# Kernel optimization log

Hardware: AMD Instinct MI355X
Metric: run time of the kernel (lower is better)

Reference implementation:

```python
import jax, jax.numpy as jnp
import numpy as np

C = 256
H = 8
D = C // H
B = 8
Q_PER = 128
KV_PER = 1024
NQ = B * Q_PER
NKV = B * KV_PER
NEG = -10000.0
MASK_EPS = 1e-6
RMS_EPS = float(np.finfo(np.float32).eps)  # torch RMSNorm default eps=None -> finfo eps


def _rms(x, w):
    return x * jax.lax.rsqrt(jnp.mean(x * x, axis=-1, keepdims=True) + RMS_EPS) * w


def _mlp(x, w1, b1, w2, b2):
    h = jax.nn.gelu(x @ w1.T + b1, approximate=False)  # torch nn.GELU is exact
    return h @ w2.T + b2


def _sdpa(qh, kh, vh, mask, scale):
    # qh [H, Nq, D], kh/vh [H, Nk, D], mask [Nq, Nk] additive
    s = jnp.einsum('hqd,hkd->hqk', qh, kh) * scale + mask[None]
    return jnp.einsum('hqk,hkd->hqd', jax.nn.softmax(s, axis=-1), vh)


def _heads(x):
    return x.reshape(-1, H, D).transpose(1, 0, 2)  # [H, N, D]


def setup_inputs() -> dict:
    key = jax.random.key(0)
    ks = jax.random.split(key, 24)
    s = 0.02
    lin = lambda k, o, i: jax.random.normal(k, (o, i), jnp.float32) * s
    inp = {
        'q': jax.random.normal(ks[0], (NQ, C), jnp.float32),
        'kv': jax.random.normal(ks[1], (NKV, C), jnp.float32),
        'cu_seqlens_q': jnp.arange(B + 1, dtype=jnp.int32) * Q_PER,
        'cu_seqlens_kv': jnp.arange(B + 1, dtype=jnp.int32) * KV_PER,
        'w_norm_kv': jnp.ones((C,), jnp.float32),
        'w_norm1': jnp.ones((C,), jnp.float32),
        'w_norm2': jnp.ones((C,), jnp.float32),
        'w_norm3': jnp.ones((C,), jnp.float32),
        'wq_c': lin(ks[2], C, C), 'wk_c': lin(ks[3], C, C), 'wv_c': lin(ks[4], C, C),
        'wo_c': lin(ks[5], C, C), 'bo_c': jnp.zeros((C,), jnp.float32),
        'wq_s': lin(ks[6], C, C), 'wkv_s': lin(ks[7], 2 * C, C),
        'wo_s': lin(ks[8], C, C), 'bo_s': jnp.zeros((C,), jnp.float32),
        'w1_mlp': lin(ks[9], 4 * C, C), 'b1_mlp': jnp.zeros((4 * C,), jnp.float32),
        'w2_mlp': lin(ks[10], C, 4 * C), 'b2_mlp': jnp.zeros((C,), jnp.float32),
        'w1_mask': lin(ks[11], C, C), 'b1_mask': jnp.zeros((C,), jnp.float32),
        'w2_mask': lin(ks[12], C, C), 'b2_mask': jnp.zeros((C,), jnp.float32),
    }
    return inp


def reference(q, kv, cu_seqlens_q, cu_seqlens_kv, w_norm_kv, w_norm1, w_norm2, w_norm3,
              wq_c, wk_c, wv_c, wo_c, bo_c, wq_s, wkv_s, wo_s, bo_s,
              w1_mlp, b1_mlp, w2_mlp, b2_mlp, w1_mask, b1_mask, w2_mask, b2_mask):
    scale = D ** (-0.5)
    nq, nkv = q.shape[0], kv.shape[0]
    # segment id per packed token from cu_seqlens
    seg_q = jnp.searchsorted(cu_seqlens_q, jnp.arange(nq), side='right') - 1
    seg_kv = jnp.searchsorted(cu_seqlens_kv, jnp.arange(nkv), side='right') - 1

    kv_n = _rms(kv, w_norm_kv)

    # mask MLP -> predicted attention mask (logits z), detached log-prob mask
    m_k = _mlp(q, w1_mask, b1_mask, w2_mask, b2_mask)          # [Nq, C]
    z = m_k @ kv_n.T                                           # [Nq, Nkv]
    p_hat = jax.nn.sigmoid(z)
    same = seg_q[:, None] == seg_kv[None, :]
    attn_mask = jnp.where(same, jnp.log(jax.lax.stop_gradient(p_hat) + MASK_EPS), NEG)

    # cross-attention (pre-norm)
    q_n = _rms(q, w_norm1)
    feat = _sdpa(_heads(q_n @ wq_c.T), _heads(kv_n @ wk_c.T), _heads(kv_n @ wv_c.T),
                 attn_mask, scale)
    feat = feat.transpose(1, 0, 2).reshape(-1, C) @ wo_c.T + bo_c
    q = q + feat

    # block-diagonal self-attention over queries
    q_n = _rms(q, w_norm2)
    kv_proj = (q_n @ wkv_s.T).reshape(-1, 2, H, D)
    self_mask = jnp.where(seg_q[:, None] == seg_q[None, :], 0.0, NEG)
    feat = _sdpa(_heads(q_n @ wq_s.T),
                 kv_proj[:, 0].transpose(1, 0, 2), kv_proj[:, 1].transpose(1, 0, 2),
                 self_mask, scale)
    feat = feat.transpose(1, 0, 2).reshape(-1, C) @ wo_s.T + bo_s
    q = q + feat

    # MLP
    q = q + _mlp(_rms(q, w_norm3), w1_mlp, b1_mlp, w2_mlp, b2_mlp)
    return q
```

## Files before the change

### kernel.cpp

```cpp
#include <hip/hip_runtime.h>
#include <math.h>


#define SCALE_ATTN 0.17677669529663687f
#define RMS_EPS 1.1920929e-07f

typedef __attribute__((ext_vector_type(8))) short bh8;
typedef __attribute__((ext_vector_type(4))) float f32x4;

__device__ __forceinline__ float bf2f(unsigned short s) {
  union { float f; unsigned u; } v; v.u = ((unsigned)s) << 16; return v.f;
}
__device__ __forceinline__ unsigned short f2bf(float f) {
  union { float f; unsigned u; } v; v.f = f;
  unsigned r = v.u + 0x7FFFu + ((v.u >> 16) & 1u);
  return (unsigned short)(r >> 16);
}
__device__ __forceinline__ unsigned pack2bf(float a, float b) {
  union { float f; unsigned u; } x, y; x.f = a; y.f = b;
  return ((x.u + 0x8000u) >> 16) | ((y.u + 0x8000u) & 0xFFFF0000u);
}
__device__ __forceinline__ float gelu_exact(float x) {
  return 0.5f * x * (1.0f + erff(x * 0.70710678118654752440f));
}

struct WP { const float* p[12]; };
__global__ __launch_bounds__(256) void k_pre(
    WP wp, unsigned short* __restrict__ wbf, unsigned short* __restrict__ w2t,
    const float* __restrict__ wn1, const float* __restrict__ wn2,
    const float* __restrict__ wn3,
    const float* __restrict__ kv, const float* __restrict__ wnkv,
    const float* __restrict__ b2m, unsigned short* __restrict__ kv_n,
    float* __restrict__ tvec, unsigned short* __restrict__ q_n,
    float* __restrict__ ssq2, float* __restrict__ ssq3) {
  int bid = blockIdx.x, tid = threadIdx.x;
  if (bid < 1408) {
    long g = ((long)bid * 256 + tid) * 4;
    const float* src; long l;
    if (g < 327680)       { src = wp.p[g >> 16]; l = g & 65535; }
    else if (g < 458752)  { src = wp.p[5];  l = g - 327680; }
    else if (g < 524288)  { src = wp.p[6];  l = g - 458752; }
    else if (g < 786432)  { src = wp.p[7];  l = g - 524288; }
    else if (g < 1048576) { src = wp.p[8];  l = g - 786432; }
    else if (g < 1114112) { src = wp.p[9];  l = g - 1048576; }
    else if (g < 1179648) { src = wp.p[10]; l = g - 1114112; }
    else                  { src = wp.p[11]; l = g - 1179648; }
    float4 v = *(const float4*)(src + l);
    if (g >= 262144 && g < 458752) {
      int k = (int)(g & 255);
      v.x *= wn2[k]; v.y *= wn2[k + 1]; v.z *= wn2[k + 2]; v.w *= wn2[k + 3];
    } else if (g >= 524288 && g < 786432) {
      int k = (int)(g & 255);
      v.x *= wn3[k]; v.y *= wn3[k + 1]; v.z *= wn3[k + 2]; v.w *= wn3[k + 3];
    }
    ushort4 o;
    o.x = f2bf(v.x); o.y = f2bf(v.y); o.z = f2bf(v.z); o.w = f2bf(v.w);
    *(ushort4*)(wbf + g) = o;
  } else if (bid < 1424) {
    __shared__ float Ts[64][65];
    int t = bid - 1408, ti = t >> 2, tj = t & 3;
    const float* w2src = wp.p[10];
    int rr = tid >> 2;
#pragma unroll
    for (int j = 0; j < 4; ++j) {
      int cc = (tid & 3) * 16 + j * 4;
      float4 v = *(const float4*)(w2src + (long)(ti * 64 + rr) * 256 + tj * 64 + cc);
      Ts[rr][cc] = v.x; Ts[rr][cc + 1] = v.y;
      Ts[rr][cc + 2] = v.z; Ts[rr][cc + 3] = v.w;
    }
    __syncthreads();
#pragma unroll
    for (int j = 0; j < 4; ++j) {
      int kk = (tid & 3) * 16 + j * 4;
      ushort4 o;
      o.x = f2bf(Ts[kk][rr]); o.y = f2bf(Ts[kk + 1][rr]);
      o.z = f2bf(Ts[kk + 2][rr]); o.w = f2bf(Ts[kk + 3][rr]);
      *(ushort4*)(w2t + (long)(tj * 64 + rr) * 256 + ti * 64 + kk) = o;
    }
  } else if (bid < 3472) {
    int row = (bid - 1424) * 4 + (tid >> 6);
    int c4 = (tid & 63) * 4;
    float4 v = *(const float4*)(kv + (long)row * 256 + c4);
    float s = v.x * v.x + v.y * v.y + v.z * v.z + v.w * v.w;
#pragma unroll
    for (int off = 32; off > 0; off >>= 1) s += __shfl_xor(s, off, 64);
    float inv = rsqrtf(s * (1.0f / 256.0f) + RMS_EPS);
    float4 wn = *(const float4*)(wnkv + c4);
    float4 b2 = *(const float4*)(b2m + c4);
    float4 vn;
    vn.x = v.x * inv * wn.x; vn.y = v.y * inv * wn.y;
    vn.z = v.z * inv * wn.z; vn.w = v.w * inv * wn.w;
    ushort4 o;
    o.x = f2bf(vn.x); o.y = f2bf(vn.y); o.z = f2bf(vn.z); o.w = f2bf(vn.w);
    *(ushort4*)(kv_n + (long)row * 256 + c4) = o;
    float s2 = vn.x * b2.x + vn.y * b2.y + vn.z * b2.z + vn.w * b2.w;
#pragma unroll
    for (int off = 32; off > 0; off >>= 1) s2 += __shfl_xor(s2, off, 64);
    if ((tid & 63) == 0) tvec[row] = s2;
  } else if (bid < 3728) {
    int row = (bid - 3472) * 4 + (tid >> 6);
    int c4 = (tid & 63) * 4;
    const float* q = wp.p[11];
    float4 v = *(const float4*)(q + (long)row * 256 + c4);
    float s = v.x * v.x + v.y * v.y + v.z * v.z + v.w * v.w;
#pragma unroll
    for (int off = 32; off > 0; off >>= 1) s += __shfl_xor(s, off, 64);
    float inv = rsqrtf(s * (1.0f / 256.0f) + RMS_EPS);
    float4 wn = *(const float4*)(wn1 + c4);
    ushort4 o;
    o.x = f2bf(v.x * inv * wn.x); o.y = f2bf(v.y * inv * wn.y);
    o.z = f2bf(v.z * inv * wn.z); o.w = f2bf(v.w * inv * wn.w);
    *(ushort4*)(q_n + (long)row * 256 + c4) = o;
  } else {
    int idx = (bid - 3728) * 256 + tid;
    if (idx < 1024) ssq2[idx] = 0.f;
    else if (idx < 2048) ssq3[idx - 1024] = 0.f;
  }
}

template <int MT, int KS>
__device__ __forceinline__ void gemm_core(
    const unsigned short* __restrict__ A, const unsigned short* __restrict__ W,
    const float* bias, const float* R, const float* ssqIn, float* ssqOut,
    float* Cf, unsigned short* Cb, unsigned short* Cb2,
    int lda, int ldw, int ldc, int m0, int n0, int epi) {
  int tid = threadIdx.x, w = tid >> 6, lane = tid & 63;
  int quad = lane >> 4, c = lane & 15;
  __shared__ __align__(16) unsigned short As[2][MT * 64][40];
  __shared__ __align__(16) unsigned short Ws[2][64][40];
  f32x4 acc[MT][4];
#pragma unroll
  for (int i = 0; i < MT; ++i)
#pragma unroll
    for (int j = 0; j < 4; ++j) acc[i][j] = (f32x4){0.f, 0.f, 0.f, 0.f};
  int ar = tid >> 2, ak = (tid & 3) * 8;
  {
    int4 a0 = *(const int4*)(A + (long)(m0 + ar) * lda + ak);
    int4 a1;
    if (MT == 2) a1 = *(const int4*)(A + (long)(m0 + 64 + ar) * lda + ak);
    int4 wv = *(const int4*)(W + (long)(n0 + ar) * ldw + ak);
    *(int4*)&As[0][ar][ak] = a0;
    if (MT == 2) *(int4*)&As[0][64 + ar][ak] = a1;
    *(int4*)&Ws[0][ar][ak] = wv;
  }
  __syncthreads();
#pragma unroll
  for (int i = 0; i < KS; ++i) {
    int cur = i & 1, nxt = cur ^ 1;
    int4 na0, na1, nwv;
    if (i + 1 < KS) {
      int k0 = (i + 1) * 32;
      na0 = *(const int4*)(A + (long)(m0 + ar) * lda + k0 + ak);
      if (MT == 2)
        na1 = *(const int4*)(A + (long)(m0 + 64 + ar) * lda + k0 + ak);
      nwv = *(const int4*)(W + (long)(n0 + ar) * ldw + k0 + ak);
    }
    bh8 af[MT];
#pragma unroll
    for (int mt = 0; mt < MT; ++mt)
      af[mt] = *(const bh8*)&As[cur][w * (16 * MT) + mt * 16 + c][quad * 8];
#pragma unroll
    for (int nt = 0; nt < 4; ++nt) {
      bh8 bf = *(const bh8*)&Ws[cur][nt * 16 + c][quad * 8];
#pragma unroll
      for (int mt = 0; mt < MT; ++mt)
        acc[mt][nt] =
            __builtin_amdgcn_mfma_f32_16x16x32_bf16(af[mt], bf, acc[mt][nt], 0, 0, 0);
    }
    if (i + 1 < KS) {
      *(int4*)&As[nxt][ar][ak] = na0;
      if (MT == 2) *(int4*)&As[nxt][64 + ar][ak] = na1;
      *(int4*)&Ws[nxt][ar][ak] = nwv;
      __syncthreads();
    }
  }
  float rsum[MT][4];
#pragma unroll
  for (int mt = 0; mt < MT; ++mt)
#pragma unroll
    for (int r = 0; r < 4; ++r) rsum[mt][r] = 0.f;
#pragma unroll
  for (int mt = 0; mt < MT; ++mt)
#pragma unroll
    for (int nt = 0; nt < 4; ++nt)
#pragma unroll
      for (int r = 0; r < 4; ++r) {
        int m = m0 + w * (16 * MT) + mt * 16 + quad * 4 + r;
        int n = n0 + nt * 16 + c;
        float v = acc[mt][nt][r];
        long ci = (long)m * ldc + n;
        if (epi == 1) {
          if (bias) v += bias[n];
          Cb[ci] = f2bf(gelu_exact(v));
        } else if (epi == 5) {
          Cb[ci] = f2bf(v);
        } else if (epi == 3) {
          if (bias) v += bias[n];
          Cb[ci] = f2bf(1.0f / (1.0f + __expf(-v)) + 1e-6f);
        } else if (epi == 2) {
          if (bias) v += bias[n];
          v += R[ci];
          Cf[ci] = v;
          if (Cb2) Cb2[ci] = f2bf(v);
          rsum[mt][r] += v * v;
        } else if (epi == 6) {
          v *= rsqrtf(ssqIn[m] * (1.0f / 256.0f) + RMS_EPS);
          if (bias) v += bias[n];
          Cb[ci] = f2bf(gelu_exact(v));
        } else {
          v *= rsqrtf(ssqIn[m] * (1.0f / 256.0f) + RMS_EPS);
          Cb[ci] = f2bf(v);
        }
      }
  if (epi == 2 && ssqOut) {
#pragma unroll
    for (int mt = 0; mt < MT; ++mt)
#pragma unroll
      for (int r = 0; r < 4; ++r) {
        float s = rsum[mt][r];
        s += __shfl_xor(s, 1, 64);
        s += __shfl_xor(s, 2, 64);
        s += __shfl_xor(s, 4, 64);
        s += __shfl_xor(s, 8, 64);
        if (c == 0)
          atomicAdd(&ssqOut[m0 + w * (16 * MT) + mt * 16 + quad * 4 + r], s);
      }
  }
}

template <int MT, int KS>
__global__ __launch_bounds__(256) void k_gemm(
    const unsigned short* A, const unsigned short* W,
    const float* bias, long sBh, const float* R,
    const float* ssqIn, float* ssqOut,
    float* Cf, unsigned short* Cb, unsigned short* Cb2,
    int lda, int ldw, int ldc, long sAh, long sWh, long sCh, int epi) {
  int z = blockIdx.z;
  long coff = (long)z * sCh;
  gemm_core<MT, KS>(A + (long)z * sAh, W + (long)z * sWh,
                    bias ? bias + (long)z * sBh : nullptr, R, ssqIn, ssqOut,
                    Cf ? Cf + coff : nullptr, Cb ? Cb + coff : nullptr, Cb2,
                    lda, ldw, ldc, blockIdx.y * (MT * 64), blockIdx.x * 64, epi);
}

struct G4 {
  const unsigned short* A; const unsigned short* W;
  const float* bias; float* Cf; unsigned short* Cb;
  int lda, ldw, ldc, epi, nx, blkStart;
};
struct G4x { G4 g[4]; };
__global__ __launch_bounds__(256) void k_gemm4(G4x d) {
  int z = blockIdx.x;
  int i = 3;
  while (i > 0 && z < d.g[i].blkStart) --i;
  const G4& g = d.g[i];
  int local = z - g.blkStart;
  int by = local / g.nx, bx = local - by * g.nx;
  gemm_core<2, 8>(g.A, g.W, g.bias, nullptr, nullptr, nullptr,
                  g.Cf, g.Cb, nullptr, g.lda, g.ldw, g.ldc,
                  by * 128, bx * 64, g.epi);
}

__global__ __launch_bounds__(256) void k_gemm_cmb(
    const float* __restrict__ partL, const float* __restrict__ partO,
    const unsigned short* __restrict__ W, const float* __restrict__ bias,
    const float* __restrict__ R, float* __restrict__ ssqOut,
    float* __restrict__ Cf, unsigned short* __restrict__ Cb2) {
  int m0 = blockIdx.y * 64, n0 = blockIdx.x * 64;
  int tid = threadIdx.x, w = tid >> 6, lane = tid & 63;
  int quad = lane >> 4, c = lane & 15;
  __shared__ __align__(16) unsigned short As[2][64][40];
  __shared__ __align__(16) unsigned short Ws[2][64][40];
  __shared__ float Linv[64][8];
  int ar = tid >> 2, ak = (tid & 3) * 8;
  int b = m0 >> 7, q0 = m0 & 127;
  {
#pragma unroll
    for (int t = 0; t < 2; ++t) {
      int e = tid * 2 + t;
      int rr = e >> 3, hh = e & 7;
      const float* pl = partL + ((long)((b * 8 + hh) * 128 + q0 + rr)) * 8;
      float Ls = 0.f;
#pragma unroll
      for (int s = 0; s < 8; ++s) Ls += pl[s];
      Linv[rr][hh] = 1.0f / Ls;
    }
  }
  __syncthreads();
  auto computeA = [&](int i, uint4& pk) {
    const float* po =
        partO + (((long)((b * 8 + i) * 128 + q0 + ar)) * 8) * 32 + ak;
    float o0 = 0, o1 = 0, o2 = 0, o3 = 0, o4 = 0, o5 = 0, o6 = 0, o7 = 0;
#pragma unroll
    for (int s = 0; s < 8; ++s) {
      float4 u = *(const float4*)(po + s * 32);
      float4 v = *(const float4*)(po + s * 32 + 4);
      o0 += u.x; o1 += u.y; o2 += u.z; o3 += u.w;
      o4 += v.x; o5 += v.y; o6 += v.z; o7 += v.w;
    }
    float inv = Linv[ar][i];
    pk.x = pack2bf(o0 * inv, o1 * inv);
    pk.y = pack2bf(o2 * inv, o3 * inv);
    pk.z = pack2bf(o4 * inv, o5 * inv);
    pk.w = pack2bf(o6 * inv, o7 * inv);
  };
  f32x4 acc[4];
#pragma unroll
  for (int j = 0; j < 4; ++j) acc[j] = (f32x4){0.f, 0.f, 0.f, 0.f};
  {
    uint4 pk;
    computeA(0, pk);
    int4 wv = *(const int4*)(W + (long)(n0 + ar) * 256 + ak);
    *(uint4*)&As[0][ar][ak] = pk;
    *(int4*)&Ws[0][ar][ak] = wv;
  }
  __syncthreads();
#pragma unroll
  for (int i = 0; i < 8; ++i) {
    int cur = i & 1, nxt = cur ^ 1;
    uint4 npk;
    int4 nwv;
    if (i + 1 < 8) {
      computeA(i + 1, npk);
      nwv = *(const int4*)(W + (long)(n0 + ar) * 256 + (i + 1) * 32 + ak);
    }
    bh8 af = *(const bh8*)&As[cur][w * 16 + c][quad * 8];
#pragma unroll
    for (int nt = 0; nt < 4; ++nt) {
      bh8 bf = *(const bh8*)&Ws[cur][nt * 16 + c][quad * 8];
      acc[nt] = __builtin_amdgcn_mfma_f32_16x16x32_bf16(af, bf, acc[nt], 0, 0, 0);
    }
    if (i + 1 < 8) {
      *(uint4*)&As[nxt][ar][ak] = npk;
      *(int4*)&Ws[nxt][ar][ak] = nwv;
      __syncthreads();
    }
  }
  float rsum[4] = {0.f, 0.f, 0.f, 0.f};
#pragma unroll
  for (int nt = 0; nt < 4; ++nt)
#pragma unroll
    for (int r = 0; r < 4; ++r) {
      int m = m0 + w * 16 + quad * 4 + r;
      int n = n0 + nt * 16 + c;
      float v = acc[nt][r] + bias[n];
      long ci = (long)m * 256 + n;
      v += R[ci];
      Cf[ci] = v;
      Cb2[ci] = f2bf(v);
      rsum[r] += v * v;
    }
#pragma unroll
  for (int r = 0; r < 4; ++r) {
    float s = rsum[r];
    s += __shfl_xor(s, 1, 64);
    s += __shfl_xor(s, 2, 64);
    s += __shfl_xor(s, 4, 64);
    s += __shfl_xor(s, 8, 64);
    if (c == 0) atomicAdd(&ssqOut[m0 + w * 16 + quad * 4 + r], s);
  }
}

template <int MODE>
__global__ __launch_bounds__(256) void k_flash(
    const unsigned short* __restrict__ Qg, int ldq,
    const unsigned short* __restrict__ KVg, int ldkv, int kvRows,
    int kOff, int vOff, const unsigned short* __restrict__ maskp,
    unsigned short* __restrict__ feat,
    float* __restrict__ partL, float* __restrict__ partO) {
  int split = blockIdx.x, bh = blockIdx.y;
  int b = bh >> 3, h = bh & 7, j0 = split * 128;
  int tid = threadIdx.x;
  int w = tid >> 6, lane = tid & 63, c = lane & 15, quad = lane >> 4;
  __shared__ __align__(16) unsigned short Ks[128][40];
  __shared__ __align__(16) unsigned short Vt[32][136];
  __shared__ __align__(16) unsigned short Pt[128][136];
  const unsigned short* Qz = Qg + (long)(b * 128) * ldq + h * 32;
  const unsigned short* Kz = KVg + ((long)b * kvRows + j0) * ldkv + kOff + h * 32;
  const unsigned short* Vz = KVg + ((long)b * kvRows + j0) * ldkv + vOff + h * 32;
  bh8 Bq[2];
#pragma unroll
  for (int nt = 0; nt < 2; ++nt)
    Bq[nt] = *(const bh8*)(Qz + (long)(w * 32 + nt * 16 + c) * ldq + quad * 8);
  {
    int row = tid >> 2, part = tid & 3;
#pragma unroll
    for (int v = 0; v < 2; ++v) {
      int r2 = row + v * 64;
      *(int4*)&Ks[r2][part * 8] = *(const int4*)(Kz + (long)r2 * ldkv + part * 8);
      int4 vv = *(const int4*)(Vz + (long)r2 * ldkv + part * 8);
      unsigned short tmp[8];
      *(int4*)tmp = vv;
#pragma unroll
      for (int i = 0; i < 8; ++i) Vt[part * 8 + i][r2] = tmp[i];
    }
  }
  __syncthreads();
  f32x4 S[8][2];
#pragma unroll
  for (int mt = 0; mt < 8; ++mt)
#pragma unroll
    for (int nt = 0; nt < 2; ++nt) S[mt][nt] = (f32x4){0.f, 0.f, 0.f, 0.f};
#pragma unroll
  for (int mt = 0; mt < 8; ++mt) {
    bh8 aK = *(const bh8*)&Ks[mt * 16 + c][quad * 8];
    S[mt][0] = __builtin_amdgcn_mfma_f32_16x16x32_bf16(aK, Bq[0], S[mt][0], 0, 0, 0);
    S[mt][1] = __builtin_amdgcn_mfma_f32_16x16x32_bf16(aK, Bq[1], S[mt][1], 0, 0, 0);
  }
  float L[2];
#pragma unroll
  for (int nt = 0; nt < 2; ++nt) {
    if (MODE == 0) {
      const unsigned short* mrow =
          maskp + ((long)(b * 128 + w * 32 + nt * 16 + c)) * 1024 + j0;
#pragma unroll
      for (int mt = 0; mt < 8; ++mt) {
        uint2 mp = *(const uint2*)(mrow + mt * 16 + quad * 4);
        S[mt][nt][0] = __expf(S[mt][nt][0] * SCALE_ATTN) * bf2f((unsigned short)mp.x);
        S[mt][nt][1] = __expf(S[mt][nt][1] * SCALE_ATTN) * bf2f((unsigned short)(mp.x >> 16));
        S[mt][nt][2] = __expf(S[mt][nt][2] * SCALE_ATTN) * bf2f((unsigned short)mp.y);
        S[mt][nt][3] = __expf(S[mt][nt][3] * SCALE_ATTN) * bf2f((unsigned short)(mp.y >> 16));
      }
    } else {
#pragma unroll
      for (int mt = 0; mt < 8; ++mt)
#pragma unroll
        for (int r = 0; r < 4; ++r)
          S[mt][nt][r] = __expf(S[mt][nt][r] * SCALE_ATTN);
    }
    float rs = 0.f;
#pragma unroll
    for (int mt = 0; mt < 8; ++mt)
#pragma unroll
      for (int r = 0; r < 4; ++r) rs += S[mt][nt][r];
    rs += __shfl_xor(rs, 16, 64);
    rs += __shfl_xor(rs, 32, 64);
    L[nt] = rs;
  }
#pragma unroll
  for (int mt = 0; mt < 8; ++mt)
#pragma unroll
    for (int nt = 0; nt < 2; ++nt) {
      uint2 pk;
      pk.x = pack2bf(S[mt][nt][0], S[mt][nt][1]);
      pk.y = pack2bf(S[mt][nt][2], S[mt][nt][3]);
      *(uint2*)&Pt[w * 32 + nt * 16 + c][mt * 16 + quad * 4] = pk;
    }
  __syncthreads();
  f32x4 acc[2][2];
#pragma unroll
  for (int i = 0; i < 2; ++i)
#pragma unroll
    for (int j = 0; j < 2; ++j) acc[i][j] = (f32x4){0.f, 0.f, 0.f, 0.f};
#pragma unroll
  for (int ks = 0; ks < 4; ++ks) {
    bh8 aP0 = *(const bh8*)&Pt[w * 32 + c][ks * 32 + quad * 8];
    bh8 aP1 = *(const bh8*)&Pt[w * 32 + 16 + c][ks * 32 + quad * 8];
    bh8 bV0 = *(const bh8*)&Vt[c][ks * 32 + quad * 8];
    bh8 bV1 = *(const bh8*)&Vt[16 + c][ks * 32 + quad * 8];
    acc[0][0] = __builtin_amdgcn_mfma_f32_16x16x32_bf16(aP0, bV0, acc[0][0], 0, 0, 0);
    acc[0][1] = __builtin_amdgcn_mfma_f32_16x16x32_bf16(aP0, bV1, acc[0][1], 0, 0, 0);
    acc[1][0] = __builtin_amdgcn_mfma_f32_16x16x32_bf16(aP1, bV0, acc[1][0], 0, 0, 0);
    acc[1][1] = __builtin_amdgcn_mfma_f32_16x16x32_bf16(aP1, bV1, acc[1][1], 0, 0, 0);
  }
  if (MODE == 0) {
    if (quad == 0) {
#pragma unroll
      for (int nt = 0; nt < 2; ++nt)
        partL[((long)(bh * 128 + w * 32 + nt * 16 + c)) * 8 + split] = L[nt];
    }
#pragma unroll
    for (int mt = 0; mt < 2; ++mt)
#pragma unroll
      for (int ct = 0; ct < 2; ++ct)
#pragma unroll
        for (int r = 0; r < 4; ++r) {
          int q = w * 32 + mt * 16 + quad * 4 + r;
          partO[(((long)(bh * 128 + q)) * 8 + split) * 32 + ct * 16 + c] =
              acc[mt][ct][r];
        }
  } else {
    unsigned short* Oz = feat + (long)(b * 128) * 256 + h * 32;
#pragma unroll
    for (int mt = 0; mt < 2; ++mt)
#pragma unroll
      for (int r = 0; r < 4; ++r) {
        float linv = 1.0f / __shfl(L[mt], quad * 4 + r, 64);
        int q = w * 32 + mt * 16 + quad * 4 + r;
        Oz[(long)q * 256 + c] = f2bf(acc[mt][0][r] * linv);
        Oz[(long)q * 256 + 16 + c] = f2bf(acc[mt][1][r] * linv);
      }
  }
}

extern "C" void kernel_launch(void* const* d_in, const int* in_sizes, int n_in,
                              void* d_out, int out_size, void* d_ws, size_t ws_size,
                              hipStream_t stream) {
  const float* q        = (const float*)d_in[0];
  const float* kv       = (const float*)d_in[1];
  const float* w_norm_kv = (const float*)d_in[4];
  const float* w_norm1  = (const float*)d_in[5];
  const float* w_norm2  = (const float*)d_in[6];
  const float* w_norm3  = (const float*)d_in[7];
  const float* bo_c     = (const float*)d_in[12];
  const float* bo_s     = (const float*)d_in[16];
  const float* b1_mlp   = (const float*)d_in[18];
  const float* b2_mlp   = (const float*)d_in[20];
  const float* b1_mask  = (const float*)d_in[22];
  const float* b2_mask  = (const float*)d_in[24];
  float* out = (float*)d_out;

  unsigned char* W8 = (unsigned char*)d_ws;
  unsigned short* wbf    = (unsigned short*)(W8 + 0);
  unsigned short* w2t    = (unsigned short*)(W8 + 2883584);
  unsigned short* kv_n   = (unsigned short*)(W8 + 3014656);
  unsigned short* q_n    = (unsigned short*)(W8 + 7208960);
  unsigned short* mh     = (unsigned short*)(W8 + 7733248);
  unsigned short* kvw    = (unsigned short*)(W8 + 8257536);
  unsigned short* maskp  = (unsigned short*)(W8 + 12451840);
  float*          tvec   = (float*)(W8 + 14548992);
  unsigned short* Qc     = (unsigned short*)(W8 + 14581760);
  unsigned short* KVc    = (unsigned short*)(W8 + 15106048);
  unsigned short* QKVs   = (unsigned short*)(W8 + 23494656);
  unsigned short* feat   = (unsigned short*)(W8 + 25067520);
  unsigned short* out1_bf = (unsigned short*)(W8 + 25591808);
  unsigned short* out2_bf = (unsigned short*)(W8 + 26116096);
  float*          ssq2   = (float*)(W8 + 26640384);
  float*          ssq3   = (float*)(W8 + 26644480);
  float*          partL  = (float*)(W8 + 26648832);
  float*          partO  = (float*)(W8 + 26910976);
  unsigned short* hid    = (unsigned short*)(W8 + 35299584);

  unsigned short* wq_c_bf   = wbf;
  unsigned short* wkv_c_bf  = wbf + 65536;
  unsigned short* wo_c_bf   = wbf + 196608;
  unsigned short* wqkv_s_bf = wbf + 262144;
  unsigned short* wo_s_bf   = wbf + 458752;
  unsigned short* w1_mlp_bf = wbf + 524288;
  unsigned short* w2_mlp_bf = wbf + 786432;
  unsigned short* w1_mask_bf = wbf + 1048576;
  unsigned short* q_bf      = wbf + 1179648;

  WP wp;
  wp.p[0] = (const float*)d_in[8];  wp.p[1] = (const float*)d_in[9];
  wp.p[2] = (const float*)d_in[10]; wp.p[3] = (const float*)d_in[11];
  wp.p[4] = (const float*)d_in[13]; wp.p[5] = (const float*)d_in[14];
  wp.p[6] = (const float*)d_in[15]; wp.p[7] = (const float*)d_in[17];
  wp.p[8] = (const float*)d_in[19]; wp.p[9] = (const float*)d_in[21];
  wp.p[10] = (const float*)d_in[23]; wp.p[11] = q;
  k_pre<<<3736, 256, 0, stream>>>(wp, wbf, w2t, w_norm1, w_norm2, w_norm3,
                                  kv, w_norm_kv, b2_mask, kv_n, tvec, q_n,
                                  ssq2, ssq3);

  G4x d;
  d.g[0] = {q_bf, w1_mask_bf, b1_mask, nullptr, mh, 256, 256, 256, 1, 4, 0};
  d.g[1] = {q_n, wq_c_bf, nullptr, nullptr, Qc, 256, 256, 256, 5, 4, 32};
  d.g[2] = {kv_n, wkv_c_bf, nullptr, nullptr, KVc, 256, 256, 512, 5, 8, 64};
  d.g[3] = {kv_n, w2t, nullptr, nullptr, kvw, 256, 256, 256, 5, 4, 576};
  k_gemm4<<<832, 256, 0, stream>>>(d);

  k_gemm<1, 8><<<dim3(16, 2, 8), 256, 0, stream>>>(mh, kvw, tvec, 1024, nullptr,
      nullptr, nullptr, nullptr, maskp, nullptr,
      256, 256, 1024, 128L * 256, 1024L * 256, 128L * 1024, 3);

  k_flash<0><<<dim3(8, 64), 256, 0, stream>>>(Qc, 256, KVc, 512, 1024, 0, 256,
                                              maskp, nullptr, partL, partO);
  k_gemm_cmb<<<dim3(4, 16), 256, 0, stream>>>(partL, partO, wo_c_bf, bo_c, q,
                                              ssq2, out, out1_bf);

  k_gemm<1, 8><<<dim3(12, 16, 1), 256, 0, stream>>>(out1_bf, wqkv_s_bf, nullptr,
      0, nullptr, ssq2, nullptr, nullptr, QKVs, nullptr,
      256, 256, 768, 0, 0, 0, 7);
  k_flash<1><<<dim3(1, 64), 256, 0, stream>>>(QKVs, 768, QKVs, 768, 128, 256,
                                              512, nullptr, feat, nullptr,
                                              nullptr);
  k_gemm<1, 8><<<dim3(4, 16, 1), 256, 0, stream>>>(feat, wo_s_bf, bo_s, 0, out,
      nullptr, ssq3, out, nullptr, out2_bf, 256, 256, 256, 0, 0, 0, 2);

  k_gemm<1, 8><<<dim3(16, 16, 1), 256, 0, stream>>>(out2_bf, w1_mlp_bf, b1_mlp,
      0, nullptr, ssq3, nullptr, nullptr, hid, nullptr,
      256, 256, 1024, 0, 0, 0, 6);
  k_gemm<1, 32><<<dim3(4, 16, 1), 256, 0, stream>>>(hid, w2_mlp_bf, b2_mlp, 0,
      out, nullptr, nullptr, out, nullptr, nullptr,
      1024, 1024, 256, 0, 0, 0, 2);
}
```

Before: 213.5 us.

## Fuse mask GEMM into cross-attention and QKV projection into self-attention

The separate mask-logit GEMM is folded into the cross-attention kernel, so each block computes its sigmoid mask tile from the mask-MLP hidden and projected keys instead of reading a materialised bf16 mask. The self-attention QKV projection is fused into a per-(batch, head) attention kernel. RMS sum-of-squares are now recomputed from the bf16 A operand inside the consuming GEMM rather than accumulated with atomics, which removes the zeroing pass and the atomicAdd epilogues. GEMM epilogues become compile-time templates. The cost is redundant mask and QKV compute per block, self-attention running on only 64 blocks, and norms taken from bf16-rounded activations.

New measurement: 215.4 us. No clear change (+0.9%).

```diff
diff --git a/kernel.cpp b/kernel.cpp
--- a/kernel.cpp
+++ b/kernel.cpp
@@ -22,6 +22,18 @@
 }
 __device__ __forceinline__ float gelu_exact(float x) {
   return 0.5f * x * (1.0f + erff(x * 0.70710678118654752440f));
+}
+__device__ __forceinline__ float sum8sq(int4 v) {
+  float s = 0.f;
+  unsigned u[4] = {(unsigned)v.x, (unsigned)v.y, (unsigned)v.z, (unsigned)v.w};
+#pragma unroll
+  for (int i = 0; i < 4; ++i) {
+    union { float f; unsigned q; } lo, hi;
+    lo.q = u[i] << 16;
+    hi.q = u[i] & 0xFFFF0000u;
+    s += lo.f * lo.f + hi.f * hi.f;
+  }
+  return s;
 }
 
 struct WP { const float* p[12]; };
@@ -31,8 +43,7 @@
     const float* __restrict__ wn3,
     const float* __restrict__ kv, const float* __restrict__ wnkv,
     const float* __restrict__ b2m, unsigned short* __restrict__ kv_n,
-    float* __restrict__ tvec, unsigned short* __restrict__ q_n,
-    float* __restrict__ ssq2, float* __restrict__ ssq3) {
+    float* __restrict__ tvec, unsigned short* __restrict__ q_n) {
   int bid = blockIdx.x, tid = threadIdx.x;
   if (bid < 1408) {
     long g = ((long)bid * 256 + tid) * 4;
@@ -97,7 +108,7 @@
 #pragma unroll
     for (int off = 32; off > 0; off >>= 1) s2 += __shfl_xor(s2, off, 64);
     if ((tid & 63) == 0) tvec[row] = s2;
-  } else if (bid < 3728) {
+  } else {
     int row = (bid - 3472) * 4 + (tid >> 6);
     int c4 = (tid & 63) * 4;
     const float* q = wp.p[11];
@@ -111,34 +122,33 @@
     o.x = f2bf(v.x * inv * wn.x); o.y = f2bf(v.y * inv * wn.y);
     o.z = f2bf(v.z * inv * wn.z); o.w = f2bf(v.w * inv * wn.w);
     *(ushort4*)(q_n + (long)row * 256 + c4) = o;
-  } else {
-    int idx = (bid - 3728) * 256 + tid;
-    if (idx < 1024) ssq2[idx] = 0.f;
-    else if (idx < 2048) ssq3[idx - 1024] = 0.f;
-  }
-}
-
-template <int MT, int KS>
+  }
+}
+
+template <int MT, int KS, int EPI>
 __device__ __forceinline__ void gemm_core(
     const unsigned short* __restrict__ A, const unsigned short* __restrict__ W,
-    const float* bias, const float* R, const float* ssqIn, float* ssqOut,
+    const float* bias, const float* R,
     float* Cf, unsigned short* Cb, unsigned short* Cb2,
-    int lda, int ldw, int ldc, int m0, int n0, int epi) {
+    int lda, int ldw, int ldc, int m0, int n0) {
   int tid = threadIdx.x, w = tid >> 6, lane = tid & 63;
   int quad = lane >> 4, c = lane & 15;
   __shared__ __align__(16) unsigned short As[2][MT * 64][40];
   __shared__ __align__(16) unsigned short Ws[2][64][40];
+  __shared__ float ssqLds[64];
   f32x4 acc[MT][4];
 #pragma unroll
   for (int i = 0; i < MT; ++i)
 #pragma unroll
     for (int j = 0; j < 4; ++j) acc[i][j] = (f32x4){0.f, 0.f, 0.f, 0.f};
   int ar = tid >> 2, ak = (tid & 3) * 8;
+  float asum = 0.f;
   {
     int4 a0 = *(const int4*)(A + (long)(m0 + ar) * lda + ak);
     int4 a1;
     if (MT == 2) a1 = *(const int4*)(A + (long)(m0 + 64 + ar) * lda + ak);
     int4 wv = *(const int4*)(W + (long)(n0 + ar) * ldw + ak);
+    if (EPI == 8) asum += sum8sq(a0);
     *(int4*)&As[0][ar][ak] = a0;
     if (MT == 2) *(int4*)&As[0][64 + ar][ak] = a1;
     *(int4*)&Ws[0][ar][ak] = wv;
@@ -168,79 +178,56 @@
             __builtin_amdgcn_mfma_f32_16x16x32_bf16(af[mt], bf, acc[mt][nt], 0, 0, 0);
     }
     if (i + 1 < KS) {
+      if (EPI == 8) asum += sum8sq(na0);
       *(int4*)&As[nxt][ar][ak] = na0;
       if (MT == 2) *(int4*)&As[nxt][64 + ar][ak] = na1;
       *(int4*)&Ws[nxt][ar][ak] = nwv;
       __syncthreads();
     }
   }
-  float rsum[MT][4];
+  if (EPI == 8) {
+    asum += __shfl_xor(asum, 1, 64);
+    asum += __shfl_xor(asum, 2, 64);
+    if ((tid & 3) == 0) ssqLds[ar] = asum;
+    __syncthreads();
+  }
 #pragma unroll
   for (int mt = 0; mt < MT; ++mt)
 #pragma unroll
-    for (int r = 0; r < 4; ++r) rsum[mt][r] = 0.f;
-#pragma unroll
-  for (int mt = 0; mt < MT; ++mt)
-#pragma unroll
     for (int nt = 0; nt < 4; ++nt)
 #pragma unroll
       for (int r = 0; r < 4; ++r) {
-        int m = m0 + w * (16 * MT) + mt * 16 + quad * 4 + r;
+        int lm = w * (16 * MT) + mt * 16 + quad * 4 + r;
+        int m = m0 + lm;
         int n = n0 + nt * 16 + c;
         float v = acc[mt][nt][r];
         long ci = (long)m * ldc + n;
-        if (epi == 1) {
+        if (EPI == 1) {
           if (bias) v += bias[n];
           Cb[ci] = f2bf(gelu_exact(v));
-        } else if (epi == 5) {
+        } else if (EPI == 5) {
           Cb[ci] = f2bf(v);
-        } else if (epi == 3) {
-          if (bias) v += bias[n];
-          Cb[ci] = f2bf(1.0f / (1.0f + __expf(-v)) + 1e-6f);
-        } else if (epi == 2) {
+        } else if (EPI == 2) {
           if (bias) v += bias[n];
           v += R[ci];
           Cf[ci] = v;
           if (Cb2) Cb2[ci] = f2bf(v);
-          rsum[mt][r] += v * v;
-        } else if (epi == 6) {
-          v *= rsqrtf(ssqIn[m] * (1.0f / 256.0f) + RMS_EPS);
+        } else {
+          v *= rsqrtf(ssqLds[lm] * (1.0f / 256.0f) + RMS_EPS);
           if (bias) v += bias[n];
           Cb[ci] = f2bf(gelu_exact(v));
-        } else {
-          v *= rsqrtf(ssqIn[m] * (1.0f / 256.0f) + RMS_EPS);
-          Cb[ci] = f2bf(v);
         }
       }
-  if (epi == 2 && ssqOut) {
-#pragma unroll
-    for (int mt = 0; mt < MT; ++mt)
-#pragma unroll
-      for (int r = 0; r < 4; ++r) {
-        float s = rsum[mt][r];
-        s += __shfl_xor(s, 1, 64);
-        s += __shfl_xor(s, 2, 64);
-        s += __shfl_xor(s, 4, 64);
-        s += __shfl_xor(s, 8, 64);
-        if (c == 0)
-          atomicAdd(&ssqOut[m0 + w * (16 * MT) + mt * 16 + quad * 4 + r], s);
-      }
-  }
-}
-
-template <int MT, int KS>
+}
+
+template <int MT, int KS, int EPI>
 __global__ __launch_bounds__(256) void k_gemm(
     const unsigned short* A, const unsigned short* W,
-    const float* bias, long sBh, const float* R,
-    const float* ssqIn, float* ssqOut,
+    const float* bias, const float* R,
     float* Cf, unsigned short* Cb, unsigned short* Cb2,
-    int lda, int ldw, int ldc, long sAh, long sWh, long sCh, int epi) {
-  int z = blockIdx.z;
-  long coff = (long)z * sCh;
-  gemm_core<MT, KS>(A + (long)z * sAh, W + (long)z * sWh,
-                    bias ? bias + (long)z * sBh : nullptr, R, ssqIn, ssqOut,
-                    Cf ? Cf + coff : nullptr, Cb ? Cb + coff : nullptr, Cb2,
-                    lda, ldw, ldc, blockIdx.y * (MT * 64), blockIdx.x * 64, epi);
+    int lda, int ldw, int ldc) {
+  gemm_core<MT, KS, EPI>(A, W, bias, R, Cf, Cb, Cb2, lda, ldw, ldc,
+                         blockIdx.y * (MT * 64), blockIdx.x * 64);
 }
 
 struct G4 {
@@ -256,15 +243,147 @@
   const G4& g = d.g[i];
   int local = z - g.blkStart;
   int by = local / g.nx, bx = local - by * g.nx;
-  gemm_core<2, 8>(g.A, g.W, g.bias, nullptr, nullptr, nullptr,
-                  g.Cf, g.Cb, nullptr, g.lda, g.ldw, g.ldc,
-                  by * 128, bx * 64, g.epi);
+  if (g.epi == 1)
+    gemm_core<2, 8, 1>(g.A, g.W, g.bias, nullptr, nullptr, g.Cb, nullptr,
+                       g.lda, g.ldw, g.ldc, by * 128, bx * 64);
+  else
+    gemm_core<2, 8, 5>(g.A, g.W, g.bias, nullptr, nullptr, g.Cb, nullptr,
+                       g.lda, g.ldw, g.ldc, by * 128, bx * 64);
+}
+
+__global__ __launch_bounds__(256) void k_flash(
+    const unsigned short* __restrict__ Qg,
+    const unsigned short* __restrict__ KVg,
+    const unsigned short* __restrict__ mh,
+    const unsigned short* __restrict__ kvw,
+    const float* __restrict__ tvec,
+    float* __restrict__ partL, float* __restrict__ partO) {
+  int split = blockIdx.x, bh = blockIdx.y;
+  int b = bh >> 3, h = bh & 7, j0 = split * 128;
+  int tid = threadIdx.x;
+  int w = tid >> 6, lane = tid & 63, c = lane & 15, quad = lane >> 4;
+  __shared__ __align__(16) unsigned short Ks[128][40];
+  __shared__ __align__(16) unsigned short Vt[32][136];
+  __shared__ __align__(16) unsigned short Pt[128][136];
+  __shared__ float tvLds[128];
+  const unsigned short* Qz = Qg + (long)(b * 128) * 256 + h * 32;
+  const unsigned short* Kz = KVg + ((long)(b * 1024 + j0)) * 512 + h * 32;
+  const unsigned short* Vz = Kz + 256;
+  if (tid < 128) tvLds[tid] = tvec[b * 1024 + j0 + tid];
+  bh8 Bq[2];
+#pragma unroll
+  for (int nt = 0; nt < 2; ++nt)
+    Bq[nt] = *(const bh8*)(Qz + (long)(w * 32 + nt * 16 + c) * 256 + quad * 8);
+  {
+    int row = tid >> 2, part = tid & 3;
+#pragma unroll
+    for (int v = 0; v < 2; ++v) {
+      int r2 = row + v * 64;
+      *(int4*)&Ks[r2][part * 8] = *(const int4*)(Kz + (long)r2 * 512 + part * 8);
+      int4 vv = *(const int4*)(Vz + (long)r2 * 512 + part * 8);
+      unsigned short tmp[8];
+      *(int4*)tmp = vv;
+#pragma unroll
+      for (int i = 0; i < 8; ++i) Vt[part * 8 + i][r2] = tmp[i];
+    }
+  }
+  const unsigned short* Az = kvw + (long)(b * 1024 + j0) * 256;
+  const unsigned short* Bz = mh + (long)(b * 128) * 256;
+  f32x4 Z[8][2];
+#pragma unroll
+  for (int mt = 0; mt < 8; ++mt)
+#pragma unroll
+    for (int nt = 0; nt < 2; ++nt) Z[mt][nt] = (f32x4){0.f, 0.f, 0.f, 0.f};
+#pragma unroll
+  for (int k0 = 0; k0 < 256; k0 += 32) {
+    bh8 bz[2];
+#pragma unroll
+    for (int nt = 0; nt < 2; ++nt)
+      bz[nt] = *(const bh8*)(Bz + (long)(w * 32 + nt * 16 + c) * 256 + k0 + quad * 8);
+#pragma unroll
+    for (int mt = 0; mt < 8; ++mt) {
+      bh8 az = *(const bh8*)(Az + (long)(mt * 16 + c) * 256 + k0 + quad * 8);
+      Z[mt][0] = __builtin_amdgcn_mfma_f32_16x16x32_bf16(az, bz[0], Z[mt][0], 0, 0, 0);
+      Z[mt][1] = __builtin_amdgcn_mfma_f32_16x16x32_bf16(az, bz[1], Z[mt][1], 0, 0, 0);
+    }
+  }
+  __syncthreads();
+  f32x4 S[8][2];
+#pragma unroll
+  for (int mt = 0; mt < 8; ++mt)
+#pragma unroll
+    for (int nt = 0; nt < 2; ++nt) S[mt][nt] = (f32x4){0.f, 0.f, 0.f, 0.f};
+#pragma unroll
+  for (int mt = 0; mt < 8; ++mt) {
+    bh8 aK = *(const bh8*)&Ks[mt * 16 + c][quad * 8];
+    S[mt][0] = __builtin_amdgcn_mfma_f32_16x16x32_bf16(aK, Bq[0], S[mt][0], 0, 0, 0);
+    S[mt][1] = __builtin_amdgcn_mfma_f32_16x16x32_bf16(aK, Bq[1], S[mt][1], 0, 0, 0);
+  }
+  float L[2];
+#pragma unroll
+  for (int nt = 0; nt < 2; ++nt) {
+    float rs = 0.f;
+#pragma unroll
+    for (int mt = 0; mt < 8; ++mt)
+#pragma unroll
+      for (int r = 0; r < 4; ++r) {
+        float zz = Z[mt][nt][r] + tvLds[mt * 16 + quad * 4 + r];
+        float p = 1.0f / (1.0f + __expf(-zz)) + 1e-6f;
+        float e = __expf(S[mt][nt][r] * SCALE_ATTN) * p;
+        S[mt][nt][r] = e;
+        rs += e;
+      }
+    rs += __shfl_xor(rs, 16, 64);
+    rs += __shfl_xor(rs, 32, 64);
+    L[nt] = rs;
+  }
+#pragma unroll
+  for (int mt = 0; mt < 8; ++mt)
+#pragma unroll
+    for (int nt = 0; nt < 2; ++nt) {
+      uint2 pk;
+      pk.x = pack2bf(S[mt][nt][0], S[mt][nt][1]);
+      pk.y = pack2bf(S[mt][nt][2], S[mt][nt][3]);
+      *(uint2*)&Pt[w * 32 + nt * 16 + c][mt * 16 + quad * 4] = pk;
+    }
+  __syncthreads();
+  f32x4 acc[2][2];
+#pragma unroll
+  for (int i = 0; i < 2; ++i)
+#pragma unroll
+    for (int j = 0; j < 2; ++j) acc[i][j] = (f32x4){0.f, 0.f, 0.f, 0.f};
+#pragma unroll
+  for (int ks = 0; ks < 4; ++ks) {
+    bh8 aP0 = *(const bh8*)&Pt[w * 32 + c][ks * 32 + quad * 8];
+    bh8 aP1 = *(const bh8*)&Pt[w * 32 + 16 + c][ks * 32 + quad * 8];
+    bh8 bV0 = *(const bh8*)&Vt[c][ks * 32 + quad * 8];
+    bh8 bV1 = *(const bh8*)&Vt[16 + c][ks * 32 + quad * 8];
+    acc[0][0] = __builtin_amdgcn_mfma_f32_16x16x32_bf16(aP0, bV0, acc[0][0], 0, 0, 0);
+    acc[0][1] = __builtin_amdgcn_mfma_f32_16x16x32_bf16(aP0, bV1, acc[0][1], 0, 0, 0);
+    acc[1][0] = __builtin_amdgcn_mfma_f32_16x16x32_bf16(aP1, bV0, acc[1][0], 0, 0, 0);
+    acc[1][1] = __builtin_amdgcn_mfma_f32_16x16x32_bf16(aP1, bV1, acc[1][1], 0, 0, 0);
+  }
+  if (quad == 0) {
+#pragma unroll
+    for (int nt = 0; nt < 2; ++nt)
+      partL[((long)(bh * 128 + w * 32 + nt * 16 + c)) * 8 + split] = L[nt];
+  }
+#pragma unroll
+  for (int mt = 0; mt < 2; ++mt)
+#pragma unroll
+    for (int ct = 0; ct < 2; ++ct)
+#pragma unroll
+      for (int r = 0; r < 4; ++r) {
+        int q = w * 32 + mt * 16 + quad * 4 + r;
+        partO[(((long)(bh * 128 + q)) * 8 + split) * 32 + ct * 16 + c] =
+            acc[mt][ct][r];
+      }
 }
 
 __global__ __launch_bounds__(256) void k_gemm_cmb(
     const float* __restrict__ partL, const float* __restrict__ partO,
     const unsigned short* __restrict__ W, const float* __restrict__ bias,
-    const float* __restrict__ R, float* __restrict__ ssqOut,
+    const float* __restrict__ R,
     float* __restrict__ Cf, unsigned short* __restrict__ Cb2) {
   int m0 = blockIdx.y * 64, n0 = blockIdx.x * 64;
   int tid = threadIdx.x, w = tid >> 6, lane = tid & 63;
@@ -336,7 +455,6 @@
       __syncthreads();
     }
   }
-  float rsum[4] = {0.f, 0.f, 0.f, 0.f};
 #pragma unroll
   for (int nt = 0; nt < 4; ++nt)
 #pragma unroll
@@ -348,54 +466,75 @@
       v += R[ci];
       Cf[ci] = v;
       Cb2[ci] = f2bf(v);
-      rsum[r] += v * v;
-    }
-#pragma unroll
-  for (int r = 0; r < 4; ++r) {
-    float s = rsum[r];
-    s += __shfl_xor(s, 1, 64);
-    s += __shfl_xor(s, 2, 64);
-    s += __shfl_xor(s, 4, 64);
-    s += __shfl_xor(s, 8, 64);
-    if (c == 0) atomicAdd(&ssqOut[m0 + w * 16 + quad * 4 + r], s);
-  }
-}
-
-template <int MODE>
-__global__ __launch_bounds__(256) void k_flash(
-    const unsigned short* __restrict__ Qg, int ldq,
-    const unsigned short* __restrict__ KVg, int ldkv, int kvRows,
-    int kOff, int vOff, const unsigned short* __restrict__ maskp,
-    unsigned short* __restrict__ feat,
-    float* __restrict__ partL, float* __restrict__ partO) {
-  int split = blockIdx.x, bh = blockIdx.y;
-  int b = bh >> 3, h = bh & 7, j0 = split * 128;
-  int tid = threadIdx.x;
-  int w = tid >> 6, lane = tid & 63, c = lane & 15, quad = lane >> 4;
+    }
+}
+
+__global__ __launch_bounds__(256) void k_selfattn(
+    const unsigned short* __restrict__ X,
+    const unsigned short* __restrict__ Wqkv,
+    unsigned short* __restrict__ feat) {
+  int z = blockIdx.x, b = z >> 3, h = z & 7;
+  int tid = threadIdx.x, w = tid >> 6, lane = tid & 63;
+  int c = lane & 15, quad = lane >> 4;
+  __shared__ __align__(16) unsigned short Qs[128][40];
   __shared__ __align__(16) unsigned short Ks[128][40];
   __shared__ __align__(16) unsigned short Vt[32][136];
   __shared__ __align__(16) unsigned short Pt[128][136];
-  const unsigned short* Qz = Qg + (long)(b * 128) * ldq + h * 32;
-  const unsigned short* Kz = KVg + ((long)b * kvRows + j0) * ldkv + kOff + h * 32;
-  const unsigned short* Vz = KVg + ((long)b * kvRows + j0) * ldkv + vOff + h * 32;
+  __shared__ float ssqLds[128];
+  const unsigned short* Xz = X + (long)(b * 128) * 256;
+  int wr[6];
+  wr[0] = h * 32;       wr[1] = h * 32 + 16;
+  wr[2] = 256 + h * 32; wr[3] = 256 + h * 32 + 16;
+  wr[4] = 512 + h * 32; wr[5] = 512 + h * 32 + 16;
+  f32x4 acc[2][6];
+#pragma unroll
+  for (int i = 0; i < 2; ++i)
+#pragma unroll
+    for (int j = 0; j < 6; ++j) acc[i][j] = (f32x4){0.f, 0.f, 0.f, 0.f};
+  float asq[2] = {0.f, 0.f};
+#pragma unroll
+  for (int k0 = 0; k0 < 256; k0 += 32) {
+    bh8 af[2];
+#pragma unroll
+    for (int mt = 0; mt < 2; ++mt) {
+      af[mt] = *(const bh8*)(Xz + (long)(w * 32 + mt * 16 + c) * 256 + k0 + quad * 8);
+      asq[mt] += sum8sq(*(int4*)&af[mt]);
+    }
+#pragma unroll
+    for (int nt = 0; nt < 6; ++nt) {
+      bh8 wf = *(const bh8*)(Wqkv + (long)(wr[nt] + c) * 256 + k0 + quad * 8);
+#pragma unroll
+      for (int mt = 0; mt < 2; ++mt)
+        acc[mt][nt] =
+            __builtin_amdgcn_mfma_f32_16x16x32_bf16(af[mt], wf, acc[mt][nt], 0, 0, 0);
+    }
+  }
+#pragma unroll
+  for (int mt = 0; mt < 2; ++mt) {
+    float s = asq[mt];
+    s += __shfl_xor(s, 16, 64);
+    s += __shfl_xor(s, 32, 64);
+    if (quad == 0) ssqLds[w * 32 + mt * 16 + c] = s;
+  }
+#pragma unroll
+  for (int mt = 0; mt < 2; ++mt)
+#pragma unroll
+    for (int r = 0; r < 4; ++r) {
+      int tok = w * 32 + mt * 16 + quad * 4 + r;
+      float inv = rsqrtf(ssqLds[tok] * (1.0f / 256.0f) + RMS_EPS);
+#pragma unroll
+      for (int nt = 0; nt < 6; ++nt) {
+        unsigned short bv = f2bf(acc[mt][nt][r] * inv);
+        if (nt < 2)      Qs[tok][nt * 16 + c] = bv;
+        else if (nt < 4) Ks[tok][(nt - 2) * 16 + c] = bv;
+        else             Vt[(nt - 4) * 16 + c][tok] = bv;
+      }
+    }
+  __syncthreads();
   bh8 Bq[2];
 #pragma unroll
   for (int nt = 0; nt < 2; ++nt)
-    Bq[nt] = *(const bh8*)(Qz + (long)(w * 32 + nt * 16 + c) * ldq + quad * 8);
-  {
-    int row = tid >> 2, part = tid & 3;
-#pragma unroll
-    for (int v = 0; v < 2; ++v) {
-      int r2 = row + v * 64;
-      *(int4*)&Ks[r2][part * 8] = *(const int4*)(Kz + (long)r2 * ldkv + part * 8);
-      int4 vv = *(const int4*)(Vz + (long)r2 * ldkv + part * 8);
-      unsigned short tmp[8];
-      *(int4*)tmp = vv;
-#pragma unroll
-      for (int i = 0; i < 8; ++i) Vt[part * 8 + i][r2] = tmp[i];
-    }
-  }
-  __syncthreads();
+    Bq[nt] = *(const bh8*)&Qs[w * 32 + nt * 16 + c][quad * 8];
   f32x4 S[8][2];
 #pragma unroll
   for (int mt = 0; mt < 8; ++mt)
@@ -410,29 +549,15 @@
   float L[2];
 #pragma unroll
   for (int nt = 0; nt < 2; ++nt) {
-    if (MODE == 0) {
-      const unsigned short* mrow =
-          maskp + ((long)(b * 128 + w * 32 + nt * 16 + c)) * 1024 + j0;
-#pragma unroll
-      for (int mt = 0; mt < 8; ++mt) {
-        uint2 mp = *(const uint2*)(mrow + mt * 16 + quad * 4);
-        S[mt][nt][0] = __expf(S[mt][nt][0] * SCALE_ATTN) * bf2f((unsigned short)mp.x);
-        S[mt][nt][1] = __expf(S[mt][nt][1] * SCALE_ATTN) * bf2f((unsigned short)(mp.x >> 16));
-        S[mt][nt][2] = __expf(S[mt][nt][2] * SCALE_ATTN) * bf2f((unsigned short)mp.y);
-        S[mt][nt][3] = __expf(S[mt][nt][3] * SCALE_ATTN) * bf2f((unsigned short)(mp.y >> 16));
+    float rs = 0.f;
+#pragma unroll
+    for (int mt = 0; mt < 8; ++mt)
+#pragma unroll
+      for (int r = 0; r < 4; ++r) {
+        float e = __expf(S[mt][nt][r] * SCALE_ATTN);
+        S[mt][nt][r] = e;
+        rs += e;
       }
-    } else {
-#pragma unroll
-      for (int mt = 0; mt < 8; ++mt)
-#pragma unroll
-        for (int r = 0; r < 4; ++r)
-          S[mt][nt][r] = __expf(S[mt][nt][r] * SCALE_ATTN);
-    }
-    float rs = 0.f;
-#pragma unroll
-    for (int mt = 0; mt < 8; ++mt)
-#pragma unroll
-      for (int r = 0; r < 4; ++r) rs += S[mt][nt][r];
     rs += __shfl_xor(rs, 16, 64);
     rs += __shfl_xor(rs, 32, 64);
     L[nt] = rs;
@@ -447,50 +572,32 @@
       *(uint2*)&Pt[w * 32 + nt * 16 + c][mt * 16 + quad * 4] = pk;
     }
   __syncthreads();
-  f32x4 acc[2][2];
+  f32x4 o[2][2];
 #pragma unroll
   for (int i = 0; i < 2; ++i)
 #pragma unroll
-    for (int j = 0; j < 2; ++j) acc[i][j] = (f32x4){0.f, 0.f, 0.f, 0.f};
+    for (int j = 0; j < 2; ++j) o[i][j] = (f32x4){0.f, 0.f, 0.f, 0.f};
 #pragma unroll
   for (int ks = 0; ks < 4; ++ks) {
     bh8 aP0 = *(const bh8*)&Pt[w * 32 + c][ks * 32 + quad * 8];
     bh8 aP1 = *(const bh8*)&Pt[w * 32 + 16 + c][ks * 32 + quad * 8];
     bh8 bV0 = *(const bh8*)&Vt[c][ks * 32 + quad * 8];
     bh8 bV1 = *(const bh8*)&Vt[16 + c][ks * 32 + quad * 8];
-    acc[0][0] = __builtin_amdgcn_mfma_f32_16x16x32_bf16(aP0, bV0, acc[0][0], 0, 0, 0);
-    acc[0][1] = __builtin_amdgcn_mfma_f32_16x16x32_bf16(aP0, bV1, acc[0][1], 0, 0, 0);
-    acc[1][0] = __builtin_amdgcn_mfma_f32_16x16x32_bf16(aP1, bV0, acc[1][0], 0, 0, 0);
-    acc[1][1] = __builtin_amdgcn_mfma_f32_16x16x32_bf16(aP1, bV1, acc[1][1], 0, 0, 0);
-  }
-  if (MODE == 0) {
-    if (quad == 0) {
-#pragma unroll
-      for (int nt = 0; nt < 2; ++nt)
-        partL[((long)(bh * 128 + w * 32 + nt * 16 + c)) * 8 + split] = L[nt];
-    }
-#pragma unroll
-    for (int mt = 0; mt < 2; ++mt)
-#pragma unroll
-      for (int ct = 0; ct < 2; ++ct)
-#pragma unroll
-        for (int r = 0; r < 4; ++r) {
-          int q = w * 32 + mt * 16 + quad * 4 + r;
-          partO[(((long)(bh * 128 + q)) * 8 + split) * 32 + ct * 16 + c] =
-              acc[mt][ct][r];
-        }
-  } else {
-    unsigned short* Oz = feat + (long)(b * 128) * 256 + h * 32;
-#pragma unroll
-    for (int mt = 0; mt < 2; ++mt)
-#pragma unroll
-      for (int r = 0; r < 4; ++r) {
-        float linv = 1.0f / __shfl(L[mt], quad * 4 + r, 64);
-        int q = w * 32 + mt * 16 + quad * 4 + r;
-        Oz[(long)q * 256 + c] = f2bf(acc[mt][0][r] * linv);
-        Oz[(long)q * 256 + 16 + c] = f2bf(acc[mt][1][r] * linv);
-      }
-  }
+    o[0][0] = __builtin_amdgcn_mfma_f32_16x16x32_bf16(aP0, bV0, o[0][0], 0, 0, 0);
+    o[0][1] = __builtin_amdgcn_mfma_f32_16x16x32_bf16(aP0, bV1, o[0][1], 0, 0, 0);
+    o[1][0] = __builtin_amdgcn_mfma_f32_16x16x32_bf16(aP1, bV0, o[1][0], 0, 0, 0);
+    o[1][1] = __builtin_amdgcn_mfma_f32_16x16x32_bf16(aP1, bV1, o[1][1], 0, 0, 0);
+  }
+  unsigned short* Oz = feat + (long)(b * 128) * 256 + h * 32;
+#pragma unroll
+  for (int mt = 0; mt < 2; ++mt)
+#pragma unroll
+    for (int r = 0; r < 4; ++r) {
+      float linv = 1.0f / __shfl(L[mt], quad * 4 + r, 64);
+      int q = w * 32 + mt * 16 + quad * 4 + r;
+      Oz[(long)q * 256 + c] = f2bf(o[mt][0][r] * linv);
+      Oz[(long)q * 256 + 16 + c] = f2bf(o[mt][1][r] * linv);
+    }
 }
 
 extern "C" void kernel_launch(void* const* d_in, const int* in_sizes, int n_in,
@@ -517,16 +624,12 @@
   unsigned short* q_n    = (unsigned short*)(W8 + 7208960);
   unsigned short* mh     = (unsigned short*)(W8 + 7733248);
   unsigned short* kvw    = (unsigned short*)(W8 + 8257536);
-  unsigned short* maskp  = (unsigned short*)(W8 + 12451840);
   float*          tvec   = (float*)(W8 + 14548992);
   unsigned short* Qc     = (unsigned short*)(W8 + 14581760);
   unsigned short* KVc    = (unsigned short*)(W8 + 15106048);
-  unsigned short* QKVs   = (unsigned short*)(W8 + 23494656);
   unsigned short* feat   = (unsigned short*)(W8 + 25067520);
   unsigned short* out1_bf = (unsigned short*)(W8 + 25591808);
   unsigned short* out2_bf = (unsigned short*)(W8 + 26116096);
-  float*          ssq2   = (float*)(W8 + 26640384);
-  float*          ssq3   = (float*)(W8 + 26644480);
   float*          partL  = (float*)(W8 + 26648832);
   float*          partO  = (float*)(W8 + 26910976);
   unsigned short* hid    = (unsigned short*)(W8 + 35299584);
@@ -548,9 +651,8 @@
   wp.p[6] = (const float*)d_in[15]; wp.p[7] = (const float*)d_in[17];
   wp.p[8] = (const float*)d_in[19]; wp.p[9] = (const float*)d_in[21];
   wp.p[10] = (const float*)d_in[23]; wp.p[11] = q;
-  k_pre<<<3736, 256, 0, stream>>>(wp, wbf, w2t, w_norm1, w_norm2, w_norm3,
-                                  kv, w_norm_kv, b2_mask, kv_n, tvec, q_n,
-                                  ssq2, ssq3);
+  k_pre<<<3728, 256, 0, stream>>>(wp, wbf, w2t, w_norm1, w_norm2, w_norm3,
+                                  kv, w_norm_kv, b2_mask, kv_n, tvec, q_n);
 
   G4x d;
   d.g[0] = {q_bf, w1_mask_bf, b1_mask, nullptr, mh, 256, 256, 256, 1, 4, 0};
@@ -559,28 +661,20 @@
   d.g[3] = {kv_n, w2t, nullptr, nullptr, kvw, 256, 256, 256, 5, 4, 576};
   k_gemm4<<<832, 256, 0, stream>>>(d);
 
-  k_gemm<1, 8><<<dim3(16, 2, 8), 256, 0, stream>>>(mh, kvw, tvec, 1024, nullptr,
-      nullptr, nullptr, nullptr, maskp, nullptr,
-      256, 256, 1024, 128L * 256, 1024L * 256, 128L * 1024, 3);
-
-  k_flash<0><<<dim3(8, 64), 256, 0, stream>>>(Qc, 256, KVc, 512, 1024, 0, 256,
-                                              maskp, nullptr, partL, partO);
+  k_flash<<<dim3(8, 64), 256, 0, stream>>>(Qc, KVc, mh, kvw, tvec,
+                                           partL, partO);
+
   k_gemm_cmb<<<dim3(4, 16), 256, 0, stream>>>(partL, partO, wo_c_bf, bo_c, q,
-                                              ssq2, out, out1_bf);
-
-  k_gemm<1, 8><<<dim3(12, 16, 1), 256, 0, stream>>>(out1_bf, wqkv_s_bf, nullptr,
-      0, nullptr, ssq2, nullptr, nullptr, QKVs, nullptr,
-      256, 256, 768, 0, 0, 0, 7);
-  k_flash<1><<<dim3(1, 64), 256, 0, stream>>>(QKVs, 768, QKVs, 768, 128, 256,
-                                              512, nullptr, feat, nullptr,
-                                              nullptr);
-  k_gemm<1, 8><<<dim3(4, 16, 1), 256, 0, stream>>>(feat, wo_s_bf, bo_s, 0, out,
-      nullptr, ssq3, out, nullptr, out2_bf, 256, 256, 256, 0, 0, 0, 2);
-
-  k_gemm<1, 8><<<dim3(16, 16, 1), 256, 0, stream>>>(out2_bf, w1_mlp_bf, b1_mlp,
-      0, nullptr, ssq3, nullptr, nullptr, hid, nullptr,
-      256, 256, 1024, 0, 0, 0, 6);
-  k_gemm<1, 32><<<dim3(4, 16, 1), 256, 0, stream>>>(hid, w2_mlp_bf, b2_mlp, 0,
-      out, nullptr, nullptr, out, nullptr, nullptr,
-      1024, 1024, 256, 0, 0, 0, 2);
-}
+                                              out, out1_bf);
+
+  k_selfattn<<<64, 256, 0, stream>>>(out1_bf, wqkv_s_bf, feat);
+
+  k_gemm<1, 8, 2><<<dim3(4, 16), 256, 0, stream>>>(
+      feat, wo_s_bf, bo_s, out, out, nullptr, out2_bf, 256, 256, 256);
+
+  k_gemm<1, 8, 8><<<dim3(16, 16), 256, 0, stream>>>(
+      out2_bf, w1_mlp_bf, b1_mlp, nullptr, nullptr, hid, nullptr, 256, 256, 1024);
+
+  k_gemm<1, 32, 2><<<dim3(4, 16), 256, 0, stream>>>(
+      hid, w2_mlp_bf, b2_mlp, out, out, nullptr, nullptr, 1024, 1024, 256);
+}
```
